# Performance work log

Hardware: AMD Instinct MI355X
Metric: run time of the kernel (lower is better)

## Reference

```python
import jax, jax.numpy as jnp
import numpy as np

MASK_RATIO = 0.02
N2V_W, WAV_W, TV_W = 1.0, 0.2, 0.01
THRESHOLD = 50.0
LEVELS = 3


def setup_inputs() -> dict:
    key = jax.random.key(0)
    k1, k2, k3 = jax.random.split(key, 3)
    shape = (64, 1, 512, 512)
    pred = jax.random.uniform(k1, shape, dtype=jnp.float32)
    noisy_input = jax.random.uniform(k2, shape, dtype=jnp.float32)
    # N2V random blind-spot mask (torch.rand_like(pred) < mask_ratio)
    mask = jax.random.uniform(k3, shape, dtype=jnp.float32) < MASK_RATIO
    return {"pred": pred, "noisy_input": noisy_input, "mask": mask}


def haar_dwt2(x):
    # x: [B, H, W] with H, W even. Single-level 2D Haar DWT (pywt 'haar').
    a = x[:, 0::2, 0::2]
    b = x[:, 0::2, 1::2]
    c = x[:, 1::2, 0::2]
    d = x[:, 1::2, 1::2]
    ll = (a + b + c + d) * 0.5
    ch = (a + b - c - d) * 0.5  # horizontal detail
    cv = (a - b + c - d) * 0.5  # vertical detail
    cd = (a - b - c + d) * 0.5  # diagonal detail
    return ll, ch, cv, cd


def _level_l1(c, thr):
    # L1 between coeff and its (detached) soft-thresholded version
    target = jax.lax.stop_gradient(jnp.sign(c) * jnp.maximum(jnp.abs(c) - thr, 0.0))
    return jnp.mean(jnp.abs(c - target))


def reference(pred, noisy_input, mask):
    p = jnp.clip(pred, 0.0, 1.0)

    # --- Noise2Void masked L1 ---
    m = mask.astype(p.dtype)
    n2v = jnp.sum(jnp.abs(p - noisy_input) * m) / jnp.maximum(jnp.sum(m), 1.0)

    # --- Wavelet sparsity (multi-level Haar, soft-threshold targets) ---
    x = p[:, 0]  # [B, H, W]
    details = []  # finest first
    for _ in range(LEVELS):
        x, ch, cv, cd = haar_dwt2(x)
        details.append((ch, cv, cd))
    wav = jnp.asarray(0.0, dtype=p.dtype)
    for level_idx in range(1, LEVELS + 1):  # level_idx=1 -> coarsest (wavedec2 order)
        ch, cv, cd = details[LEVELS - level_idx]
        thr = (THRESHOLD / (2.0 ** (level_idx - 1))) / 255.0
        lvl = (_level_l1(ch, thr) + _level_l1(cv, thr) + _level_l1(cd, thr)) / 3.0
        wav = wav + (1.0 / level_idx) * lvl

    # --- Total variation ---
    tv = jnp.mean(jnp.abs(p[:, :, 1:, :] - p[:, :, :-1, :])) + \
         jnp.mean(jnp.abs(p[:, :, :, 1:] - p[:, :, :, :-1]))

    return N2V_W * n2v + WAV_W * wav + TV_W * tv
```

## Files before the change

kernel.cpp:

```cpp
#include <hip/hip_runtime.h>

#define NIMG 64
#define H 512
#define W 512

constexpr float THR_64  = 50.0f / 255.0f;
constexpr float THR_128 = 50.0f / 2.0f / 255.0f;
constexpr float THR_256 = 50.0f / 4.0f / 255.0f;

__device__ __forceinline__ float wave_sum(float v) {
#pragma unroll
    for (int o = 32; o > 0; o >>= 1) v += __shfl_down(v, o, 64);
    return v;
}

__device__ __forceinline__ float clip01(float x) {
    return fminf(fmaxf(x, 0.0f), 1.0f);
}

__device__ __forceinline__ float4 clip4(float4 p) {
    p.x = clip01(p.x); p.y = clip01(p.y); p.z = clip01(p.z); p.w = clip01(p.w);
    return p;
}

__global__ __launch_bounds__(256) void kA(const float* __restrict__ pred,
                                          const float* __restrict__ noisy,
                                          const int* __restrict__ mask,
                                          float4* __restrict__ pA,
                                          float* __restrict__ ll1) {
    __shared__ float red[4][4];

    const int tid = threadIdx.x;
    const int lane = tid & 63;
    const int wv = tid >> 6;
    const int bid = blockIdx.x;
    const int n = bid >> 5;
    const int tile = bid & 31;

    float n2v = 0.0f, msum = 0.0f, tv = 0.0f, wav = 0.0f;

#pragma unroll
    for (int k = 0; k < 4; ++k) {
        const int idx = (k << 2) + wv;
        const int prl = idx >> 1;
        const int h = idx & 1;
        const int pr = (tile << 3) + prl;
        const int r0 = pr << 1;
        const int col = (h << 8) + (lane << 2);
        const size_t base = (size_t)n * (H * W) + (size_t)r0 * W + col;

        float4 p0 = *reinterpret_cast<const float4*>(pred + base);
        float4 p1 = *reinterpret_cast<const float4*>(pred + base + W);
        float4 nz0 = *reinterpret_cast<const float4*>(noisy + base);
        float4 nz1 = *reinterpret_cast<const float4*>(noisy + base + W);
        int4 mk0 = *reinterpret_cast<const int4*>(mask + base);
        int4 mk1 = *reinterpret_cast<const int4*>(mask + base + W);
        float4 hal = make_float4(0, 0, 0, 0);
        const bool has_halo = (pr > 0);
        if (has_halo) hal = clip4(*reinterpret_cast<const float4*>(pred + base - W));
        float e0 = 0.0f, e1 = 0.0f;
        const bool edge = (h == 0) && (lane == 63);
        if (edge) {
            e0 = clip01(pred[base + 4]);
            e1 = clip01(pred[base + W + 4]);
        }

        p0 = clip4(p0); p1 = clip4(p1);

        {
            float m;
            m = mk0.x ? 1.f : 0.f; n2v += fabsf(p0.x - nz0.x) * m; msum += m;
            m = mk0.y ? 1.f : 0.f; n2v += fabsf(p0.y - nz0.y) * m; msum += m;
            m = mk0.z ? 1.f : 0.f; n2v += fabsf(p0.z - nz0.z) * m; msum += m;
            m = mk0.w ? 1.f : 0.f; n2v += fabsf(p0.w - nz0.w) * m; msum += m;
            m = mk1.x ? 1.f : 0.f; n2v += fabsf(p1.x - nz1.x) * m; msum += m;
            m = mk1.y ? 1.f : 0.f; n2v += fabsf(p1.y - nz1.y) * m; msum += m;
            m = mk1.z ? 1.f : 0.f; n2v += fabsf(p1.z - nz1.z) * m; msum += m;
            m = mk1.w ? 1.f : 0.f; n2v += fabsf(p1.w - nz1.w) * m; msum += m;
        }

        tv += fabsf(p0.y - p0.x) + fabsf(p0.z - p0.y) + fabsf(p0.w - p0.z);
        tv += fabsf(p1.y - p1.x) + fabsf(p1.z - p1.y) + fabsf(p1.w - p1.z);
        float nxt0 = __shfl_down(p0.x, 1, 64);
        float nxt1 = __shfl_down(p1.x, 1, 64);
        if (lane < 63) tv += fabsf(nxt0 - p0.w) + fabsf(nxt1 - p1.w);
        if (edge) tv += fabsf(e0 - p0.w) + fabsf(e1 - p1.w);
        tv += fabsf(p1.x - p0.x) + fabsf(p1.y - p0.y)
            + fabsf(p1.z - p0.z) + fabsf(p1.w - p0.w);
        if (has_halo) {
            tv += fabsf(p0.x - hal.x) + fabsf(p0.y - hal.y)
                + fabsf(p0.z - hal.z) + fabsf(p0.w - hal.w);
        }

        float a, b, c, d, ch, cv, cd, ll0, ll1v;
        a = p0.x; b = p0.y; c = p1.x; d = p1.y;
        ll0 = (a + b + c + d) * 0.5f;
        ch = (a + b - c - d) * 0.5f; cv = (a - b + c - d) * 0.5f; cd = (a - b - c + d) * 0.5f;
        wav += fminf(fabsf(ch), THR_256) + fminf(fabsf(cv), THR_256) + fminf(fabsf(cd), THR_256);
        a = p0.z; b = p0.w; c = p1.z; d = p1.w;
        ll1v = (a + b + c + d) * 0.5f;
        ch = (a + b - c - d) * 0.5f; cv = (a - b + c - d) * 0.5f; cd = (a - b - c + d) * 0.5f;
        wav += fminf(fabsf(ch), THR_256) + fminf(fabsf(cv), THR_256) + fminf(fabsf(cd), THR_256);

        *reinterpret_cast<float2*>(ll1 + (size_t)n * 65536 + (size_t)pr * 256 +
                                   (h << 7) + (lane << 1)) = make_float2(ll0, ll1v);
    }

    float v0 = wave_sum(n2v);
    float v1 = wave_sum(msum);
    float v2 = wave_sum(tv);
    float v3 = wave_sum(wav);
    if (lane == 0) { red[wv][0] = v0; red[wv][1] = v1; red[wv][2] = v2; red[wv][3] = v3; }
    __syncthreads();
    if (tid == 0) {
        pA[bid] = make_float4(red[0][0] + red[1][0] + red[2][0] + red[3][0],
                              red[0][1] + red[1][1] + red[2][1] + red[3][1],
                              red[0][2] + red[1][2] + red[2][2] + red[3][2],
                              red[0][3] + red[1][3] + red[2][3] + red[3][3]);
    }
}

__global__ __launch_bounds__(256) void kBC(const float* __restrict__ ll1,
                                           float2* __restrict__ pBC) {
    __shared__ float ll2[32][129];
    __shared__ float red2[4], red3[4];

    const int tid = threadIdx.x;
    const int lane = tid & 63, wv = tid >> 6;
    const int bid = blockIdx.x;
    const int n = bid >> 2;
    const int s = bid & 3;
    const float* src = ll1 + (size_t)n * 65536 + (size_t)(s << 6) * 256;

    float wav2 = 0.0f;
#pragma unroll
    for (int i = 0; i < 16; ++i) {
        int q = (i << 8) + tid;
        int qr = q >> 7;
        int qc = q & 127;
        float2 top = *reinterpret_cast<const float2*>(src + (2 * qr) * 256 + 2 * qc);
        float2 bot = *reinterpret_cast<const float2*>(src + (2 * qr + 1) * 256 + 2 * qc);
        float a = top.x, b = top.y, c = bot.x, d = bot.y;
        float ch = (a + b - c - d) * 0.5f;
        float cv = (a - b + c - d) * 0.5f;
        float cd = (a - b - c + d) * 0.5f;
        wav2 += fminf(fabsf(ch), THR_128) + fminf(fabsf(cv), THR_128) + fminf(fabsf(cd), THR_128);
        ll2[qr][qc] = (a + b + c + d) * 0.5f;
    }
    __syncthreads();

    float wav3 = 0.0f;
#pragma unroll
    for (int i = 0; i < 4; ++i) {
        int q = (i << 8) + tid;
        int qr = q >> 6;
        int qc = q & 63;
        float a = ll2[2 * qr][2 * qc],     b = ll2[2 * qr][2 * qc + 1];
        float c = ll2[2 * qr + 1][2 * qc], d = ll2[2 * qr + 1][2 * qc + 1];
        float ch = (a + b - c - d) * 0.5f;
        float cv = (a - b + c - d) * 0.5f;
        float cd = (a - b - c + d) * 0.5f;
        wav3 += fminf(fabsf(ch), THR_64) + fminf(fabsf(cv), THR_64) + fminf(fabsf(cd), THR_64);
    }

    float v2 = wave_sum(wav2);
    float v3 = wave_sum(wav3);
    if (lane == 0) { red2[wv] = v2; red3[wv] = v3; }
    __syncthreads();
    if (tid == 0) {
        pBC[bid] = make_float2(red2[0] + red2[1] + red2[2] + red2[3],
                               red3[0] + red3[1] + red3[2] + red3[3]);
    }
}

__global__ __launch_bounds__(256) void kD(const float4* __restrict__ pA,
                                          const float2* __restrict__ pBC,
                                          float* __restrict__ out) {
    __shared__ float red[4][6];
    const int tid = threadIdx.x;
    const int lane = tid & 63, wv = tid >> 6;

    float s0 = 0, s1 = 0, s2 = 0, s3 = 0, s4 = 0, s5 = 0;
#pragma unroll
    for (int j = 0; j < 8; ++j) {
        float4 v = pA[tid + (j << 8)];
        s0 += v.x; s1 += v.y; s2 += v.z; s3 += v.w;
    }
    {
        float2 w = pBC[tid];
        s4 += w.x; s5 += w.y;
    }
    s0 = wave_sum(s0); s1 = wave_sum(s1); s2 = wave_sum(s2);
    s3 = wave_sum(s3); s4 = wave_sum(s4); s5 = wave_sum(s5);
    if (lane == 0) {
        red[wv][0] = s0; red[wv][1] = s1; red[wv][2] = s2;
        red[wv][3] = s3; red[wv][4] = s4; red[wv][5] = s5;
    }
    __syncthreads();
    if (tid == 0) {
        float a0 = red[0][0] + red[1][0] + red[2][0] + red[3][0];
        float a1 = red[0][1] + red[1][1] + red[2][1] + red[3][1];
        float a2 = red[0][2] + red[1][2] + red[2][2] + red[3][2];
        float a3 = red[0][3] + red[1][3] + red[2][3] + red[3][3];
        float a4 = red[0][4] + red[1][4] + red[2][4] + red[3][4];
        float a5 = red[0][5] + red[1][5] + red[2][5] + red[3][5];
        float n2v = a0 / fmaxf(a1, 1.0f);
        float tv = a2 / 16744448.0f;
        float wav = a3 * (1.0f / 37748736.0f)
                  + a4 * (1.0f / 6291456.0f)
                  + a5 * (1.0f / 786432.0f);
        out[0] = 1.0f * n2v + 0.2f * wav + 0.01f * tv;
    }
}

extern "C" void kernel_launch(void* const* d_in, const int* in_sizes, int n_in,
                              void* d_out, int out_size, void* d_ws, size_t ws_size,
                              hipStream_t stream) {
    (void)in_sizes; (void)n_in; (void)out_size; (void)ws_size;
    const float* pred  = (const float*)d_in[0];
    const float* noisy = (const float*)d_in[1];
    const int*   mask  = (const int*)d_in[2];

    float4* pA  = (float4*)d_ws;
    float2* pBC = (float2*)((char*)d_ws + 2048 * 16);
    float*  ll1 = (float*)((char*)d_ws + 65536);

    kA<<<NIMG * 32, 256, 0, stream>>>(pred, noisy, mask, pA, ll1);
    kBC<<<NIMG * 4, 256, 0, stream>>>(ll1, pBC);
    kD<<<1, 256, 0, stream>>>(pA, pBC, (float*)d_out);
}
```

Before: 202.1 us.

## Fuse second Haar level into first-pass kernel using 4-row wave tiles

```diff
diff --git a/kernel.cpp b/kernel.cpp
--- a/kernel.cpp
+++ b/kernel.cpp
@@ -23,158 +23,184 @@
     return p;
 }
 
-__global__ __launch_bounds__(256) void kA(const float* __restrict__ pred,
-                                          const float* __restrict__ noisy,
-                                          const int* __restrict__ mask,
-                                          float4* __restrict__ pA,
-                                          float* __restrict__ ll1) {
-    __shared__ float red[4][4];
+__global__ __launch_bounds__(256, 4) void kA(const float* __restrict__ pred,
+                                             const float* __restrict__ noisy,
+                                             const int* __restrict__ mask,
+                                             float4* __restrict__ pA,
+                                             float* __restrict__ pW2,
+                                             float* __restrict__ ll2) {
+    __shared__ float red[4][5];
 
     const int tid = threadIdx.x;
     const int lane = tid & 63;
     const int wv = tid >> 6;
-    const int bid = blockIdx.x;
-    const int n = bid >> 5;
-    const int tile = bid & 31;
-
-    float n2v = 0.0f, msum = 0.0f, tv = 0.0f, wav = 0.0f;
-
-#pragma unroll
-    for (int k = 0; k < 4; ++k) {
-        const int idx = (k << 2) + wv;
-        const int prl = idx >> 1;
-        const int h = idx & 1;
-        const int pr = (tile << 3) + prl;
-        const int r0 = pr << 1;
-        const int col = (h << 8) + (lane << 2);
-        const size_t base = (size_t)n * (H * W) + (size_t)r0 * W + col;
-
-        float4 p0 = *reinterpret_cast<const float4*>(pred + base);
-        float4 p1 = *reinterpret_cast<const float4*>(pred + base + W);
-        float4 nz0 = *reinterpret_cast<const float4*>(noisy + base);
-        float4 nz1 = *reinterpret_cast<const float4*>(noisy + base + W);
-        int4 mk0 = *reinterpret_cast<const int4*>(mask + base);
-        int4 mk1 = *reinterpret_cast<const int4*>(mask + base + W);
-        float4 hal = make_float4(0, 0, 0, 0);
-        const bool has_halo = (pr > 0);
-        if (has_halo) hal = clip4(*reinterpret_cast<const float4*>(pred + base - W));
-        float e0 = 0.0f, e1 = 0.0f;
-        const bool edge = (h == 0) && (lane == 63);
-        if (edge) {
-            e0 = clip01(pred[base + 4]);
-            e1 = clip01(pred[base + W + 4]);
-        }
-
-        p0 = clip4(p0); p1 = clip4(p1);
-
-        {
-            float m;
-            m = mk0.x ? 1.f : 0.f; n2v += fabsf(p0.x - nz0.x) * m; msum += m;
-            m = mk0.y ? 1.f : 0.f; n2v += fabsf(p0.y - nz0.y) * m; msum += m;
-            m = mk0.z ? 1.f : 0.f; n2v += fabsf(p0.z - nz0.z) * m; msum += m;
-            m = mk0.w ? 1.f : 0.f; n2v += fabsf(p0.w - nz0.w) * m; msum += m;
-            m = mk1.x ? 1.f : 0.f; n2v += fabsf(p1.x - nz1.x) * m; msum += m;
-            m = mk1.y ? 1.f : 0.f; n2v += fabsf(p1.y - nz1.y) * m; msum += m;
-            m = mk1.z ? 1.f : 0.f; n2v += fabsf(p1.z - nz1.z) * m; msum += m;
-            m = mk1.w ? 1.f : 0.f; n2v += fabsf(p1.w - nz1.w) * m; msum += m;
-        }
-
-        tv += fabsf(p0.y - p0.x) + fabsf(p0.z - p0.y) + fabsf(p0.w - p0.z);
-        tv += fabsf(p1.y - p1.x) + fabsf(p1.z - p1.y) + fabsf(p1.w - p1.z);
-        float nxt0 = __shfl_down(p0.x, 1, 64);
-        float nxt1 = __shfl_down(p1.x, 1, 64);
-        if (lane < 63) tv += fabsf(nxt0 - p0.w) + fabsf(nxt1 - p1.w);
-        if (edge) tv += fabsf(e0 - p0.w) + fabsf(e1 - p1.w);
-        tv += fabsf(p1.x - p0.x) + fabsf(p1.y - p0.y)
-            + fabsf(p1.z - p0.z) + fabsf(p1.w - p0.w);
-        if (has_halo) {
-            tv += fabsf(p0.x - hal.x) + fabsf(p0.y - hal.y)
-                + fabsf(p0.z - hal.z) + fabsf(p0.w - hal.w);
-        }
-
-        float a, b, c, d, ch, cv, cd, ll0, ll1v;
+    const int w = (blockIdx.x << 2) + wv;
+    const int n = w >> 8;
+    const int rem = w & 255;
+    const int q = rem >> 1;
+    const int h = rem & 1;
+    const int r0 = q << 2;
+    const int col = (h << 8) + (lane << 2);
+    const size_t base = (size_t)n * (H * W) + (size_t)r0 * W + col;
+    const bool has_halo = (q > 0);
+    const size_t baseH = has_halo ? (base - W) : base;
+
+    float4 p0 = *reinterpret_cast<const float4*>(pred + base);
+    float4 p1 = *reinterpret_cast<const float4*>(pred + base + W);
+    float4 p2 = *reinterpret_cast<const float4*>(pred + base + 2 * W);
+    float4 p3 = *reinterpret_cast<const float4*>(pred + base + 3 * W);
+    float4 hl = *reinterpret_cast<const float4*>(pred + baseH);
+    float4 nz0 = *reinterpret_cast<const float4*>(noisy + base);
+    float4 nz1 = *reinterpret_cast<const float4*>(noisy + base + W);
+    float4 nz2 = *reinterpret_cast<const float4*>(noisy + base + 2 * W);
+    float4 nz3 = *reinterpret_cast<const float4*>(noisy + base + 3 * W);
+    int4 mk0 = *reinterpret_cast<const int4*>(mask + base);
+    int4 mk1 = *reinterpret_cast<const int4*>(mask + base + W);
+    int4 mk2 = *reinterpret_cast<const int4*>(mask + base + 2 * W);
+    int4 mk3 = *reinterpret_cast<const int4*>(mask + base + 3 * W);
+    float e0 = 0.f, e1 = 0.f, e2 = 0.f, e3 = 0.f;
+    const bool edge = (h == 0) && (lane == 63);
+    if (edge) {
+        e0 = clip01(pred[base + 4]);
+        e1 = clip01(pred[base + W + 4]);
+        e2 = clip01(pred[base + 2 * W + 4]);
+        e3 = clip01(pred[base + 3 * W + 4]);
+    }
+
+    p0 = clip4(p0); p1 = clip4(p1); p2 = clip4(p2); p3 = clip4(p3);
+    hl = clip4(hl);
+
+    float n2v = 0.0f, msum = 0.0f;
+    {
+        float m;
+        m = mk0.x ? 1.f : 0.f; n2v += fabsf(p0.x - nz0.x) * m; msum += m;
+        m = mk0.y ? 1.f : 0.f; n2v += fabsf(p0.y - nz0.y) * m; msum += m;
+        m = mk0.z ? 1.f : 0.f; n2v += fabsf(p0.z - nz0.z) * m; msum += m;
+        m = mk0.w ? 1.f : 0.f; n2v += fabsf(p0.w - nz0.w) * m; msum += m;
+        m = mk1.x ? 1.f : 0.f; n2v += fabsf(p1.x - nz1.x) * m; msum += m;
+        m = mk1.y ? 1.f : 0.f; n2v += fabsf(p1.y - nz1.y) * m; msum += m;
+        m = mk1.z ? 1.f : 0.f; n2v += fabsf(p1.z - nz1.z) * m; msum += m;
+        m = mk1.w ? 1.f : 0.f; n2v += fabsf(p1.w - nz1.w) * m; msum += m;
+        m = mk2.x ? 1.f : 0.f; n2v += fabsf(p2.x - nz2.x) * m; msum += m;
+        m = mk2.y ? 1.f : 0.f; n2v += fabsf(p2.y - nz2.y) * m; msum += m;
+        m = mk2.z ? 1.f : 0.f; n2v += fabsf(p2.z - nz2.z) * m; msum += m;
+        m = mk2.w ? 1.f : 0.f; n2v += fabsf(p2.w - nz2.w) * m; msum += m;
+        m = mk3.x ? 1.f : 0.f; n2v += fabsf(p3.x - nz3.x) * m; msum += m;
+        m = mk3.y ? 1.f : 0.f; n2v += fabsf(p3.y - nz3.y) * m; msum += m;
+        m = mk3.z ? 1.f : 0.f; n2v += fabsf(p3.z - nz3.z) * m; msum += m;
+        m = mk3.w ? 1.f : 0.f; n2v += fabsf(p3.w - nz3.w) * m; msum += m;
+    }
+
+    float tv = 0.0f;
+    tv += fabsf(p0.y - p0.x) + fabsf(p0.z - p0.y) + fabsf(p0.w - p0.z);
+    tv += fabsf(p1.y - p1.x) + fabsf(p1.z - p1.y) + fabsf(p1.w - p1.z);
+    tv += fabsf(p2.y - p2.x) + fabsf(p2.z - p2.y) + fabsf(p2.w - p2.z);
+    tv += fabsf(p3.y - p3.x) + fabsf(p3.z - p3.y) + fabsf(p3.w - p3.z);
+    float nx0 = __shfl_down(p0.x, 1, 64);
+    float nx1 = __shfl_down(p1.x, 1, 64);
+    float nx2 = __shfl_down(p2.x, 1, 64);
+    float nx3 = __shfl_down(p3.x, 1, 64);
+    if (lane < 63) {
+        tv += fabsf(nx0 - p0.w) + fabsf(nx1 - p1.w)
+            + fabsf(nx2 - p2.w) + fabsf(nx3 - p3.w);
+    }
+    if (edge) {
+        tv += fabsf(e0 - p0.w) + fabsf(e1 - p1.w)
+            + fabsf(e2 - p2.w) + fabsf(e3 - p3.w);
+    }
+    tv += fabsf(p1.x - p0.x) + fabsf(p1.y - p0.y) + fabsf(p1.z - p0.z) + fabsf(p1.w - p0.w);
+    tv += fabsf(p2.x - p1.x) + fabsf(p2.y - p1.y) + fabsf(p2.z - p1.z) + fabsf(p2.w - p1.w);
+    tv += fabsf(p3.x - p2.x) + fabsf(p3.y - p2.y) + fabsf(p3.z - p2.z) + fabsf(p3.w - p2.w);
+    if (has_halo) {
+        tv += fabsf(p0.x - hl.x) + fabsf(p0.y - hl.y)
+            + fabsf(p0.z - hl.z) + fabsf(p0.w - hl.w);
+    }
+
+    float wav1 = 0.0f;
+    float llA0, llA1, llB0, llB1;
+    {
+        float a, b, c, d, ch, cv, cd;
         a = p0.x; b = p0.y; c = p1.x; d = p1.y;
-        ll0 = (a + b + c + d) * 0.5f;
-        ch = (a + b - c - d) * 0.5f; cv = (a - b + c - d) * 0.5f; cd = (a - b - c + d) * 0.5f;
-        wav += fminf(fabsf(ch), THR_256) + fminf(fabsf(cv), THR_256) + fminf(fabsf(cd), THR_256);
+        llA0 = (a + b + c + d) * 0.5f;
+        ch = (a + b - c - d) * 0.5f; cv = (a - b + c - d) * 0.5f; cd = (a - b - c + d) * 0.5f;
+        wav1 += fminf(fabsf(ch), THR_256) + fminf(fabsf(cv), THR_256) + fminf(fabsf(cd), THR_256);
         a = p0.z; b = p0.w; c = p1.z; d = p1.w;
-        ll1v = (a + b + c + d) * 0.5f;
-        ch = (a + b - c - d) * 0.5f; cv = (a - b + c - d) * 0.5f; cd = (a - b - c + d) * 0.5f;
-        wav += fminf(fabsf(ch), THR_256) + fminf(fabsf(cv), THR_256) + fminf(fabsf(cd), THR_256);
-
-        *reinterpret_cast<float2*>(ll1 + (size_t)n * 65536 + (size_t)pr * 256 +
-                                   (h << 7) + (lane << 1)) = make_float2(ll0, ll1v);
+        llA1 = (a + b + c + d) * 0.5f;
+        ch = (a + b - c - d) * 0.5f; cv = (a - b + c - d) * 0.5f; cd = (a - b - c + d) * 0.5f;
+        wav1 += fminf(fabsf(ch), THR_256) + fminf(fabsf(cv), THR_256) + fminf(fabsf(cd), THR_256);
+        a = p2.x; b = p2.y; c = p3.x; d = p3.y;
+        llB0 = (a + b + c + d) * 0.5f;
+        ch = (a + b - c - d) * 0.5f; cv = (a - b + c - d) * 0.5f; cd = (a - b - c + d) * 0.5f;
+        wav1 += fminf(fabsf(ch), THR_256) + fminf(fabsf(cv), THR_256) + fminf(fabsf(cd), THR_256);
+        a = p2.z; b = p2.w; c = p3.z; d = p3.w;
+        llB1 = (a + b + c + d) * 0.5f;
+        ch = (a + b - c - d) * 0.5f; cv = (a - b + c - d) * 0.5f; cd = (a - b - c + d) * 0.5f;
+        wav1 += fminf(fabsf(ch), THR_256) + fminf(fabsf(cv), THR_256) + fminf(fabsf(cd), THR_256);
+    }
+
+    float wav2;
+    {
+        float a = llA0, b = llA1, c = llB0, d = llB1;
+        float ll2v = (a + b + c + d) * 0.5f;
+        float ch = (a + b - c - d) * 0.5f;
+        float cv = (a - b + c - d) * 0.5f;
+        float cd = (a - b - c + d) * 0.5f;
+        wav2 = fminf(fabsf(ch), THR_128) + fminf(fabsf(cv), THR_128) + fminf(fabsf(cd), THR_128);
+        ll2[(size_t)n * 16384 + (size_t)q * 128 + (h << 6) + lane] = ll2v;
     }
 
     float v0 = wave_sum(n2v);
     float v1 = wave_sum(msum);
     float v2 = wave_sum(tv);
-    float v3 = wave_sum(wav);
-    if (lane == 0) { red[wv][0] = v0; red[wv][1] = v1; red[wv][2] = v2; red[wv][3] = v3; }
+    float v3 = wave_sum(wav1);
+    float v4 = wave_sum(wav2);
+    if (lane == 0) {
+        red[wv][0] = v0; red[wv][1] = v1; red[wv][2] = v2;
+        red[wv][3] = v3; red[wv][4] = v4;
+    }
     __syncthreads();
     if (tid == 0) {
-        pA[bid] = make_float4(red[0][0] + red[1][0] + red[2][0] + red[3][0],
-                              red[0][1] + red[1][1] + red[2][1] + red[3][1],
-                              red[0][2] + red[1][2] + red[2][2] + red[3][2],
-                              red[0][3] + red[1][3] + red[2][3] + red[3][3]);
-    }
-}
-
-__global__ __launch_bounds__(256) void kBC(const float* __restrict__ ll1,
-                                           float2* __restrict__ pBC) {
-    __shared__ float ll2[32][129];
-    __shared__ float red2[4], red3[4];
-
+        pA[blockIdx.x] = make_float4(red[0][0] + red[1][0] + red[2][0] + red[3][0],
+                                     red[0][1] + red[1][1] + red[2][1] + red[3][1],
+                                     red[0][2] + red[1][2] + red[2][2] + red[3][2],
+                                     red[0][3] + red[1][3] + red[2][3] + red[3][3]);
+        pW2[blockIdx.x] = red[0][4] + red[1][4] + red[2][4] + red[3][4];
+    }
+}
+
+__global__ __launch_bounds__(256) void kC(const float* __restrict__ ll2,
+                                          float* __restrict__ pC) {
+    __shared__ float red[4];
     const int tid = threadIdx.x;
     const int lane = tid & 63, wv = tid >> 6;
     const int bid = blockIdx.x;
-    const int n = bid >> 2;
-    const int s = bid & 3;
-    const float* src = ll1 + (size_t)n * 65536 + (size_t)(s << 6) * 256;
-
-    float wav2 = 0.0f;
+    const int n = bid >> 1;
+    const int s = bid & 1;
+    const float* src = ll2 + (size_t)n * 16384;
+
+    float wav3 = 0.0f;
 #pragma unroll
-    for (int i = 0; i < 16; ++i) {
-        int q = (i << 8) + tid;
-        int qr = q >> 7;
-        int qc = q & 127;
-        float2 top = *reinterpret_cast<const float2*>(src + (2 * qr) * 256 + 2 * qc);
-        float2 bot = *reinterpret_cast<const float2*>(src + (2 * qr + 1) * 256 + 2 * qc);
+    for (int i = 0; i < 8; ++i) {
+        int u = (i << 8) + tid;
+        int qr = (s << 5) + (u >> 6);
+        int qc = u & 63;
+        float2 top = *reinterpret_cast<const float2*>(src + (2 * qr) * 128 + 2 * qc);
+        float2 bot = *reinterpret_cast<const float2*>(src + (2 * qr + 1) * 128 + 2 * qc);
         float a = top.x, b = top.y, c = bot.x, d = bot.y;
         float ch = (a + b - c - d) * 0.5f;
         float cv = (a - b + c - d) * 0.5f;
         float cd = (a - b - c + d) * 0.5f;
-        wav2 += fminf(fabsf(ch), THR_128) + fminf(fabsf(cv), THR_128) + fminf(fabsf(cd), THR_128);
-        ll2[qr][qc] = (a + b + c + d) * 0.5f;
-    }
+        wav3 += fminf(fabsf(ch), THR_64) + fminf(fabsf(cv), THR_64) + fminf(fabsf(cd), THR_64);
+    }
+    float v = wave_sum(wav3);
+    if (lane == 0) red[wv] = v;
     __syncthreads();
-
-    float wav3 = 0.0f;
-#pragma unroll
-    for (int i = 0; i < 4; ++i) {
-        int q = (i << 8) + tid;
-        int qr = q >> 6;
-        int qc = q & 63;
-        float a = ll2[2 * qr][2 * qc],     b = ll2[2 * qr][2 * qc + 1];
-        float c = ll2[2 * qr + 1][2 * qc], d = ll2[2 * qr + 1][2 * qc + 1];
-        float ch = (a + b - c - d) * 0.5f;
-        float cv = (a - b + c - d) * 0.5f;
-        float cd = (a - b - c + d) * 0.5f;
-        wav3 += fminf(fabsf(ch), THR_64) + fminf(fabsf(cv), THR_64) + fminf(fabsf(cd), THR_64);
-    }
-
-    float v2 = wave_sum(wav2);
-    float v3 = wave_sum(wav3);
-    if (lane == 0) { red2[wv] = v2; red3[wv] = v3; }
-    __syncthreads();
-    if (tid == 0) {
-        pBC[bid] = make_float2(red2[0] + red2[1] + red2[2] + red2[3],
-                               red3[0] + red3[1] + red3[2] + red3[3]);
-    }
+    if (tid == 0) pC[bid] = red[0] + red[1] + red[2] + red[3];
 }
 
 __global__ __launch_bounds__(256) void kD(const float4* __restrict__ pA,
-                                          const float2* __restrict__ pBC,
+                                          const float* __restrict__ pW2,
+                                          const float* __restrict__ pC,
                                           float* __restrict__ out) {
     __shared__ float red[4][6];
     const int tid = threadIdx.x;
@@ -182,14 +208,13 @@
 
     float s0 = 0, s1 = 0, s2 = 0, s3 = 0, s4 = 0, s5 = 0;
 #pragma unroll
-    for (int j = 0; j < 8; ++j) {
+    for (int j = 0; j < 16; ++j) {
         float4 v = pA[tid + (j << 8)];
         s0 += v.x; s1 += v.y; s2 += v.z; s3 += v.w;
-    }
-    {
-        float2 w = pBC[tid];
-        s4 += w.x; s5 += w.y;
-    }
+        s4 += pW2[tid + (j << 8)];
+    }
+    if (tid < 128) s5 = pC[tid];
+
     s0 = wave_sum(s0); s1 = wave_sum(s1); s2 = wave_sum(s2);
     s3 = wave_sum(s3); s4 = wave_sum(s4); s5 = wave_sum(s5);
     if (lane == 0) {
@@ -222,10 +247,11 @@
     const int*   mask  = (const int*)d_in[2];
 
     float4* pA  = (float4*)d_ws;
-    float2* pBC = (float2*)((char*)d_ws + 2048 * 16);
-    float*  ll1 = (float*)((char*)d_ws + 65536);
-
-    kA<<<NIMG * 32, 256, 0, stream>>>(pred, noisy, mask, pA, ll1);
-    kBC<<<NIMG * 4, 256, 0, stream>>>(ll1, pBC);
-    kD<<<1, 256, 0, stream>>>(pA, pBC, (float*)d_out);
-}
+    float*  pW2 = (float*)((char*)d_ws + 65536);
+    float*  pC  = (float*)((char*)d_ws + 81920);
+    float*  ll2 = (float*)((char*)d_ws + 98304);
+
+    kA<<<4096, 256, 0, stream>>>(pred, noisy, mask, pA, pW2, ll2);
+    kC<<<128, 256, 0, stream>>>(ll2, pC);
+    kD<<<1, 256, 0, stream>>>(pA, pW2, pC, (float*)d_out);
+}
```

Result: faster. 197.5 us (-2.3%).
